# Optimization experiments

Hardware: AMD Instinct MI355X
Metric: run time of the kernel (lower is better)

Reference implementation:

```python
import jax, jax.numpy as jnp
import numpy as np

K = 3
BN_EPS = 1e-3


def setup_inputs() -> dict:
    key = jax.random.key(0)
    ks = jax.random.split(key, 13)
    B, N1, N2 = 8, 1024, 4096
    C1, C2, Cs = 256, 128, 64
    Ctot = C1 + C2 + Cs  # 448
    H = 256
    return {
        "points1": jax.random.normal(ks[0], (B, 3, N1), jnp.float32),
        "points2": jax.random.normal(ks[1], (B, 3, N2), jnp.float32),
        "features1": jax.random.normal(ks[2], (B, C1, N1), jnp.float32),
        "features2": jax.random.normal(ks[3], (B, C2, N2), jnp.float32),
        "skip_features": jax.random.normal(ks[4], (B, Cs, N2), jnp.float32),
        # 1x1 Conv2d weights are equivalent to dense matrices [out, in]
        "W1": jax.random.normal(ks[5], (H, Ctot), jnp.float32) * 0.05,
        "b1": jax.random.normal(ks[6], (H,), jnp.float32) * 0.05,
        "g1": 1.0 + jax.random.normal(ks[7], (H,), jnp.float32) * 0.05,
        "beta1": jax.random.normal(ks[8], (H,), jnp.float32) * 0.05,
        "W2": jax.random.normal(ks[9], (H, H), jnp.float32) * 0.05,
        "b2": jax.random.normal(ks[10], (H,), jnp.float32) * 0.05,
        "g2": 1.0 + jax.random.normal(ks[11], (H,), jnp.float32) * 0.05,
        "beta2": jax.random.normal(ks[12], (H,), jnp.float32) * 0.05,
    }


def _conv_bn_relu(x, W, b, g, beta):
    # x: [B, N, Cin]; 1x1 conv == dense matmul per point
    y = jnp.einsum("bnc,oc->bno", x, W) + b
    # BatchNorm2d in training mode: batch stats over (batch, spatial) per channel
    mu = jnp.mean(y, axis=(0, 1))
    var = jnp.mean(jnp.square(y - mu), axis=(0, 1))  # biased variance
    y = (y - mu) * jax.lax.rsqrt(var + BN_EPS) * g + beta
    return jax.nn.relu(y)


def reference(points1, points2, features1, features2, skip_features,
              W1, b1, g1, beta1, W2, b2, g2, beta2):
    p1 = jnp.swapaxes(points1, 1, 2)  # [B, N1, 3]
    p2 = jnp.swapaxes(points2, 1, 2)  # [B, N2, 3]
    # pairwise Euclidean distances [B, N2, N1]
    d2 = (jnp.sum(p2 * p2, -1, keepdims=True)
          + jnp.sum(p1 * p1, -1)[:, None, :]
          - 2.0 * jnp.einsum("bnd,bmd->bnm", p2, p1))
    dist = jnp.sqrt(jnp.maximum(d2, 0.0))
    # k smallest distances
    neg_top, ind = jax.lax.top_k(-dist, K)  # ind: [B, N2, K]
    dk = -neg_top
    inv = 1.0 / (dk + 1e-10)
    w = inv / jnp.sum(inv, -1, keepdims=True)  # [B, N2, K]
    f1 = jnp.swapaxes(features1, 1, 2)  # [B, N1, C1]
    gathered = jax.vmap(lambda f, i: f[i])(f1, ind)  # [B, N2, K, C1]
    new = jnp.einsum("bnkc,bnk->bnc", gathered, w)  # inverse-distance interp
    x = jnp.concatenate([new,
                         jnp.swapaxes(features2, 1, 2),
                         jnp.swapaxes(skip_features, 1, 2)], axis=-1)
    x = _conv_bn_relu(x, W1, b1, g1, beta1)
    x = _conv_bn_relu(x, W2, b2, g2, beta2)
    return jnp.swapaxes(x, 1, 2)  # [B, Cout, N2]
```

## Files before the change

kernel.cpp:

```cpp
#include <hip/hip_runtime.h>
#include <cstdint>
#include <cstddef>

#define B_    8
#define N1_   1024
#define N2_   4096
#define C1_   256
#define C2_   128
#define CS_   64
#define CT_   448
#define H_    256
#define ROWS_ (B_ * N2_)
#define XW_   192

typedef __attribute__((ext_vector_type(8))) short bf16x8;
typedef __attribute__((ext_vector_type(4))) float f32x4;
typedef unsigned short ushort_t;
typedef unsigned int   uint_t;

__device__ __forceinline__ ushort_t f2bf(float f) {
    uint_t u = __float_as_uint(f);
    u = (u + 0x7fffu + ((u >> 16) & 1u)) >> 16;
    return (ushort_t)u;
}
__device__ __forceinline__ float bf2f(ushort_t h) {
    return __uint_as_float(((uint_t)h) << 16);
}
__device__ __forceinline__ void glds16(const void* g, void* l) {
    __builtin_amdgcn_global_load_lds(
        (const __attribute__((address_space(1))) void*)g,
        (__attribute__((address_space(3))) void*)l, 16, 0, 0);
}

__device__ __forceinline__ void tile_decode(int d, int& m0, int& n0) {
    const int j = d >> 3;
    m0 = ((d & 7) * 32 + (j >> 2)) * 128;
    n0 = (j & 3) * 64;
}

__global__ __launch_bounds__(256) void fused_pre(
    const float* __restrict__ p1, const float* __restrict__ p2,
    int* __restrict__ ind, float* __restrict__ wout,
    const float* __restrict__ f1, const float* __restrict__ f2,
    const float* __restrict__ fs, const float* __restrict__ W1,
    const float* __restrict__ W2, ushort_t* __restrict__ f1t,
    ushort_t* __restrict__ x, ushort_t* __restrict__ W1b, ushort_t* __restrict__ W2b)
{
#pragma clang fp contract(off)
    __shared__ __align__(16) char smem[32000];
    const int t = threadIdx.x;
    const int bid = blockIdx.x;
    if (bid < 1024) {
        float4*   cand  = (float4*)(smem);
        float*    pvals = (float*)(smem + 16512);
        float*    thr   = (float*)(smem + 19584);
        ushort_t* lists = (ushort_t*)(smem + 19712);
        float*    pdd   = (float*)(smem + 25856);
        int*      pdi   = (int*)(smem + 28928);
        const int b  = bid >> 7;
        const int qb = (bid & 127) * 32;
        const float* pb1 = p1 + (size_t)b * 3 * N1_;
        for (int i = t; i < N1_; i += 256) {
            float X = pb1[i], Y = pb1[N1_ + i], Z = pb1[2 * N1_ + i];
            cand[i] = make_float4(X, Y, Z, (X * X + Y * Y) + Z * Z);
        }
        const int q = t & 31, split = t >> 5;
        const int n = qb + q;
        const float* pb2 = p2 + (size_t)b * 3 * N2_;
        const float ax = pb2[n], ay = pb2[N2_ + n], az = pb2[2 * N2_ + n];
        const float s2a = (ax * ax + ay * ay) + az * az;
        const float m2x = -2.0f * ax, m2y = -2.0f * ay, m2z = -2.0f * az;
        __syncthreads();
        const int ibeg = split * 128, iend = ibeg + 128;
        {
            float a0 = 3e38f, a1 = 3e38f, a2 = 3e38f;
            for (int i = ibeg; i < iend; ++i) {
                float4 c = cand[i];
                float fd = fmaf(c.x, m2x, fmaf(c.y, m2y, fmaf(c.z, m2z, s2a + c.w)));
                float o0 = a0, o1 = a1;
                a0 = fminf(o0, fd);
                a1 = __builtin_amdgcn_fmed3f(fd, o0, o1);
                a2 = __builtin_amdgcn_fmed3f(fd, o1, a2);
            }
            pvals[t * 3 + 0] = a0; pvals[t * 3 + 1] = a1; pvals[t * 3 + 2] = a2;
        }
        __syncthreads();
        if (t < 32) {
            float m0 = 3e38f, m1 = 3e38f, m2v = 3e38f;
#pragma unroll
            for (int g = 0; g < 8; ++g)
#pragma unroll
                for (int r = 0; r < 3; ++r) {
                    float v = pvals[(g * 32 + t) * 3 + r];
                    float o0 = m0, o1 = m1;
                    m0 = fminf(o0, v);
                    m1 = __builtin_amdgcn_fmed3f(v, o0, o1);
                    m2v = __builtin_amdgcn_fmed3f(v, o1, m2v);
                }
            thr[t] = m2v + 2e-3f;
        }
        __syncthreads();
        const float th = thr[q];
        ushort_t* mylist = lists + (q * 8 + split) * 12;
        int cnt = 0;
        for (int i = ibeg; i < iend; ++i) {
            float4 c = cand[i];
            float fd = fmaf(c.x, m2x, fmaf(c.y, m2y, fmaf(c.z, m2z, s2a + c.w)));
            if (fd <= th && cnt < 12) { mylist[cnt] = (ushort_t)i; cnt++; }
        }
        float e0 = 3e38f, e1 = 3e38f, e2 = 3e38f;
        int   j0 = 0, j1 = 0, j2 = 0;
        for (int k = 0; k < cnt; ++k) {
            const int i = mylist[k];
            float4 c = cand[i];
            float dot = (ax * c.x + ay * c.y) + az * c.z;
            float dd  = (s2a + c.w) - 2.0f * dot;
            float d   = sqrtf(fmaxf(dd, 0.0f));
            if (d < e0)      { e2 = e1; j2 = j1; e1 = e0; j1 = j0; e0 = d; j0 = i; }
            else if (d < e1) { e2 = e1; j2 = j1; e1 = d;  j1 = i; }
            else if (d < e2) { e2 = d;  j2 = i; }
        }
        pdd[(split * 32 + q) * 3 + 0] = e0; pdi[(split * 32 + q) * 3 + 0] = j0;
        pdd[(split * 32 + q) * 3 + 1] = e1; pdi[(split * 32 + q) * 3 + 1] = j1;
        pdd[(split * 32 + q) * 3 + 2] = e2; pdi[(split * 32 + q) * 3 + 2] = j2;
        __syncthreads();
        if (t < 32) {
            float f0 = 3e38f, f1v = 3e38f, f2v = 3e38f;
            int   k0 = 0, k1 = 0, k2 = 0;
#pragma unroll
            for (int g = 0; g < 8; ++g)
#pragma unroll
                for (int r = 0; r < 3; ++r) {
                    float d = pdd[(g * 32 + t) * 3 + r];
                    int   i = pdi[(g * 32 + t) * 3 + r];
                    if (d < f0)       { f2v = f1v; k2 = k1; f1v = f0; k1 = k0; f0 = d; k0 = i; }
                    else if (d < f1v) { f2v = f1v; k2 = k1; f1v = d;  k1 = i; }
                    else if (d < f2v) { f2v = d;  k2 = i; }
                }
            float inv0 = 1.0f / (f0 + 1e-10f);
            float inv1 = 1.0f / (f1v + 1e-10f);
            float inv2 = 1.0f / (f2v + 1e-10f);
            float s = (inv0 + inv1) + inv2;
            const size_t row = (size_t)b * N2_ + qb + t;
            wout[row * 3 + 0] = inv0 / s;
            wout[row * 3 + 1] = inv1 / s;
            wout[row * 3 + 2] = inv2 / s;
            ind[row * 3 + 0] = k0;
            ind[row * 3 + 1] = k1;
            ind[row * 3 + 2] = k2;
        }
    } else if (bid < 1536) {
        float (*tile)[65] = (float (*)[65])smem;
        const int bid2 = bid - 1024;
        const int b  = bid2 >> 6;
        const int ct = (bid2 >> 4) & 3;
        const int nt = bid2 & 15;
        const int c0 = ct * 64, n0 = nt * 64;
        const float* src = f1 + ((size_t)b * C1_ + c0) * N1_ + n0;
#pragma unroll
        for (int j = 0; j < 16; ++j) {
            int lin = j * 256 + t;
            int ci = lin >> 6, nj = lin & 63;
            tile[ci][nj] = src[(size_t)ci * N1_ + nj];
        }
        __syncthreads();
        ushort_t* dst = f1t + ((size_t)b * N1_ + n0) * C1_ + c0;
#pragma unroll
        for (int j = 0; j < 8; ++j) {
            int lin = j * 256 + t;
            int ni = lin >> 5, cjp = (lin & 31) * 2;
            uint_t u = (uint_t)f2bf(tile[cjp][ni]) | ((uint_t)f2bf(tile[cjp + 1][ni]) << 16);
            *(uint_t*)&dst[(size_t)ni * C1_ + cjp] = u;
        }
    } else if (bid < 3072) {
        float (*tile)[65] = (float (*)[65])smem;
        const int bid2 = bid - 1536;
        const int b   = bid2 / 192;
        const int rem = bid2 - b * 192;
        const int ct  = rem >> 6;
        const int nt  = rem & 63;
        const float* src;
        if (ct < 2) src = f2 + ((size_t)b * C2_ + ct * 64) * N2_;
        else        src = fs + (size_t)b * CS_ * N2_;
        const int coff = ct * 64;
        const int n0 = nt * 64;
#pragma unroll
        for (int j = 0; j < 16; ++j) {
            int lin = j * 256 + t;
            int ci = lin >> 6, nj = lin & 63;
            tile[ci][nj] = src[(size_t)ci * N2_ + n0 + nj];
        }
        __syncthreads();
#pragma unroll
        for (int j = 0; j < 8; ++j) {
            int lin = j * 256 + t;
            int ni = lin >> 5, cjp = (lin & 31) * 2;
            uint_t u = (uint_t)f2bf(tile[cjp][ni]) | ((uint_t)f2bf(tile[cjp + 1][ni]) << 16);
            *(uint_t*)&x[((size_t)b * N2_ + n0 + ni) * XW_ + coff + cjp] = u;
        }
    } else {
        const int i = (bid - 3072) * 256 + t;
        if (i < H_ * CT_) W1b[i] = f2bf(W1[i]);
        if (i < H_ * H_)  W2b[i] = f2bf(W2[i]);
    }
}

__global__ __launch_bounds__(256, 4) void gemm1_fused(
    const ushort_t* __restrict__ f1t, const int* __restrict__ ind,
    const float* __restrict__ wgt, const ushort_t* __restrict__ x2,
    const ushort_t* __restrict__ Bw, const float* __restrict__ bias,
    ushort_t* __restrict__ C, float* __restrict__ ssum, float* __restrict__ ssq)
{
    __shared__ __align__(16) ushort_t smem[12288];
    ushort_t* As = smem;
    ushort_t* Bs = smem + 8192;
    ushort_t* Cs = smem;
    const int t = threadIdx.x;
    int m0, n0;
    tile_decode(blockIdx.x, m0, n0);
    const int lane = t & 63;
    const int wv = t >> 6;
    const int wrow = wv & 1, wcol = wv >> 1;
    const int lm = lane & 15, lq = lane >> 4;
    const int lrow8  = lane >> 3;
    const int lchunk = (lane & 7) ^ lrow8;
    const int aswz = lm & 7;
    const ushort_t* gB = Bw + (size_t)(n0 + wv * 16 + lrow8) * CT_ + lchunk * 8;
    ushort_t* lB = Bs + wv * 1024;
    const ushort_t* gA = x2 + (size_t)(m0 + wv * 32 + lrow8) * XW_ + lchunk * 8;
    ushort_t* lA = As + wv * 2048;
    const int arow  = t >> 1;
    const int acolc = (t & 1) * 4;
    const size_t grow = (size_t)m0 + arow;
    const int bb_ = (int)(grow >> 12);
    const int* ip = ind + grow * 3;
    const float* wp = wgt + grow * 3;
    const ushort_t* fb = f1t + (size_t)bb_ * N1_ * C1_;
    const ushort_t* ga0 = fb + (size_t)ip[0] * C1_ + acolc * 8;
    const ushort_t* ga1 = fb + (size_t)ip[1] * C1_ + acolc * 8;
    const ushort_t* ga2 = fb + (size_t)ip[2] * C1_ + acolc * 8;
    const float w0 = wp[0], w1 = wp[1], w2 = wp[2];
    ushort_t* awr = As + arow * 64;
    const int arsw = arow & 7;
    f32x4 acc[4][2];
#pragma unroll
    for (int i = 0; i < 4; ++i)
#pragma unroll
        for (int j = 0; j < 2; ++j)
            acc[i][j] = (f32x4){0.f, 0.f, 0.f, 0.f};

    for (int k0 = 0; k0 < CT_; k0 += 64) {
        __syncthreads();
        if (k0 < 256) {
#pragma unroll
            for (int g = 0; g < 4; ++g) {
                uint4 va = *(const uint4*)(ga0 + k0 + g * 8);
                uint4 vb = *(const uint4*)(ga1 + k0 + g * 8);
                uint4 vc = *(const uint4*)(ga2 + k0 + g * 8);
                const uint_t* pa = (const uint_t*)&va;
                const uint_t* pb = (const uint_t*)&vb;
                const uint_t* pc = (const uint_t*)&vc;
                uint_t o[4];
#pragma unroll
                for (int e = 0; e < 4; ++e) {
                    float lo = w0 * bf2f((ushort_t)(pa[e] & 0xffff))
                             + w1 * bf2f((ushort_t)(pb[e] & 0xffff))
                             + w2 * bf2f((ushort_t)(pc[e] & 0xffff));
                    float hi = w0 * bf2f((ushort_t)(pa[e] >> 16))
                             + w1 * bf2f((ushort_t)(pb[e] >> 16))
                             + w2 * bf2f((ushort_t)(pc[e] >> 16));
                    o[e] = (uint_t)f2bf(lo) | ((uint_t)f2bf(hi) << 16);
                }
                *(uint4*)&awr[((acolc + g) ^ arsw) * 8] = *(uint4*)o;
            }
        } else {
#pragma unroll
            for (int g = 0; g < 4; ++g)
                glds16(gA + (k0 - 256) + g * 8 * XW_, lA + g * 512);
        }
#pragma unroll
        for (int g = 0; g < 2; ++g)
            glds16(gB + k0 + g * 8 * CT_, lB + g * 512);
        __syncthreads();
#pragma unroll
        for (int h = 0; h < 2; ++h) {
            bf16x8 af[4], bfr[2];
#pragma unroll
            for (int i = 0; i < 4; ++i)
                af[i] = *(const bf16x8*)&As[(wrow * 64 + i * 16 + lm) * 64
                                            + (((h * 4 + lq) ^ aswz)) * 8];
#pragma unroll
            for (int j = 0; j < 2; ++j)
                bfr[j] = *(const bf16x8*)&Bs[(wcol * 32 + j * 16 + lm) * 64
                                             + (((h * 4 + lq) ^ aswz)) * 8];
#pragma unroll
            for (int i = 0; i < 4; ++i)
#pragma unroll
                for (int j = 0; j < 2; ++j)
                    acc[i][j] = __builtin_amdgcn_mfma_f32_16x16x32_bf16(af[i], bfr[j], acc[i][j], 0, 0, 0);
        }
    }
    __syncthreads();
#pragma unroll
    for (int j = 0; j < 2; ++j) {
        const int gn_l = wcol * 32 + j * 16 + lm;
        const int gn   = n0 + gn_l;
        const float bb = bias[gn];
        float ps = 0.0f, pq = 0.0f;
#pragma unroll
        for (int i = 0; i < 4; ++i) {
            const int row_l = wrow * 64 + i * 16 + lq * 4;
            f32x4 v = acc[i][j];
#pragma unroll
            for (int r = 0; r < 4; ++r) {
                float val = v[r] + bb;
                ps += val;
                pq += val * val;
                float vo = __shfl_xor(val, 1);
                uint_t packed = (lm & 1)
                    ? ((uint_t)f2bf(vo)  | ((uint_t)f2bf(val) << 16))
                    : ((uint_t)f2bf(val) | ((uint_t)f2bf(vo)  << 16));
                if ((lm & 1) == 0)
                    *(uint_t*)&Cs[(row_l + r) * 72 + (gn_l & ~1)] = packed;
            }
        }
        ps += __shfl_xor(ps, 16); pq += __shfl_xor(pq, 16);
        ps += __shfl_xor(ps, 32); pq += __shfl_xor(pq, 32);
        if (lane < 16) {
            atomicAdd(&ssum[gn], ps);
            atomicAdd(&ssq[gn], pq);
        }
    }
    __syncthreads();
    const int srow = t >> 3;
    const int scol = (t & 7) * 8;
#pragma unroll
    for (int rep = 0; rep < 4; ++rep) {
        const int row = srow + rep * 32;
        uint4 v = *(const uint4*)&Cs[row * 72 + scol];
        *(uint4*)(C + (size_t)(m0 + row) * H_ + n0 + scol) = v;
    }
}

__global__ __launch_bounds__(256, 4) void gemm2_fused(
    const ushort_t* __restrict__ A, const ushort_t* __restrict__ Bw,
    const float* __restrict__ bias,
    const float* __restrict__ s1, const float* __restrict__ q1,
    const float* __restrict__ g1, const float* __restrict__ be1,
    ushort_t* __restrict__ C, float* __restrict__ ssum, float* __restrict__ ssq)
{
    __shared__ __align__(16) ushort_t smem[15360];
    ushort_t* As0 = smem;
    ushort_t* As1 = smem + 5120;
    ushort_t* Bs  = smem + 10240;
    float*    sc  = (float*)(smem + 14336);
    float*    sh  = (float*)(smem + 14848);
    ushort_t* Cs  = smem;
    const int t = threadIdx.x;
    int m0, n0;
    tile_decode(blockIdx.x, m0, n0);
    const int lane = t & 63;
    const int wv = t >> 6;
    const int wrow = wv & 1, wcol = wv >> 1;
    const int lm = lane & 15, lq = lane >> 4;
    const int lrow8  = lane >> 3;
    const int lchunk = (lane & 7) ^ lrow8;
    const int aswz = lm & 7;
    const int arow = t >> 1, acol = (t & 1) * 32;
    {
        const float invN = 1.0f / (float)ROWS_;
        float mu  = s1[t] * invN;
        float var = q1[t] * invN - mu * mu;
        float s   = rsqrtf(var + 1e-3f) * g1[t];
        sc[t] = s;
        sh[t] = be1[t] - mu * s;
    }
    const ushort_t* gB = Bw + (size_t)(n0 + wv * 16 + lrow8) * H_ + lchunk * 8;
    ushort_t* lB = Bs + wv * 1024;
    const ushort_t* gA = A + (size_t)(m0 + arow) * H_ + acol;
    ushort_t* As_t = (t & 1) ? As1 : As0;
    f32x4 acc[4][2];
#pragma unroll
    for (int i = 0; i < 4; ++i)
#pragma unroll
        for (int j = 0; j < 2; ++j)
            acc[i][j] = (f32x4){0.f, 0.f, 0.f, 0.f};

    for (int k0 = 0; k0 < H_; k0 += 64) {
        uint4 av[4];
#pragma unroll
        for (int g = 0; g < 4; ++g)
            av[g] = *(const uint4*)(gA + k0 + g * 8);
        __syncthreads();
#pragma unroll
        for (int g = 0; g < 2; ++g)
            glds16(gB + k0 + g * 8 * H_, lB + g * 512);
#pragma unroll
        for (int g = 0; g < 4; ++g) {
            const uint_t* wsrc = (const uint_t*)&av[g];
            uint_t o[4];
#pragma unroll
            for (int e = 0; e < 4; ++e) {
                const int cb = k0 + acol + g * 8 + 2 * e;
                float lo = __uint_as_float(wsrc[e] << 16);
                float hi = __uint_as_float(wsrc[e] & 0xffff0000u);
                float r0 = fmaxf(fmaf(lo, sc[cb],     sh[cb]),     0.0f);
                float r1 = fmaxf(fmaf(hi, sc[cb + 1], sh[cb + 1]), 0.0f);
                o[e] = (uint_t)f2bf(r0) | ((uint_t)f2bf(r1) << 16);
            }
            *(uint4*)&As_t[arow * 40 + g * 8] = *(uint4*)o;
        }
        __syncthreads();
#pragma unroll
        for (int h = 0; h < 2; ++h) {
            const ushort_t* Ah = h ? As1 : As0;
            bf16x8 af[4], bfr[2];
#pragma unroll
            for (int i = 0; i < 4; ++i)
                af[i] = *(const bf16x8*)&Ah[(wrow * 64 + i * 16 + lm) * 40 + lq * 8];
#pragma unroll
            for (int j = 0; j < 2; ++j)
                bfr[j] = *(const bf16x8*)&Bs[(wcol * 32 + j * 16 + lm) * 64
                                             + (((h * 4 + lq) ^ aswz)) * 8];
#pragma unroll
            for (int i = 0; i < 4; ++i)
#pragma unroll
                for (int j = 0; j < 2; ++j)
                    acc[i][j] = __builtin_amdgcn_mfma_f32_16x16x32_bf16(af[i], bfr[j], acc[i][j], 0, 0, 0);
        }
    }
    __syncthreads();
#pragma unroll
    for (int j = 0; j < 2; ++j) {
        const int gn_l = wcol * 32 + j * 16 + lm;
        const int gn   = n0 + gn_l;
        const float bb = bias[gn];
        float ps = 0.0f, pq = 0.0f;
#pragma unroll
        for (int i = 0; i < 4; ++i) {
            const int row_l = wrow * 64 + i * 16 + lq * 4;
            f32x4 v = acc[i][j];
#pragma unroll
            for (int r = 0; r < 4; ++r) {
                float val = v[r] + bb;
                ps += val;
                pq += val * val;
                float vo = __shfl_xor(val, 1);
                uint_t packed = (lm & 1)
                    ? ((uint_t)f2bf(vo)  | ((uint_t)f2bf(val) << 16))
                    : ((uint_t)f2bf(val) | ((uint_t)f2bf(vo)  << 16));
                if ((lm & 1) == 0)
                    *(uint_t*)&Cs[(row_l + r) * 72 + (gn_l & ~1)] = packed;
            }
        }
        ps += __shfl_xor(ps, 16); pq += __shfl_xor(pq, 16);
        ps += __shfl_xor(ps, 32); pq += __shfl_xor(pq, 32);
        if (lane < 16) {
            atomicAdd(&ssum[gn], ps);
            atomicAdd(&ssq[gn], pq);
        }
    }
    __syncthreads();
    const int srow = t >> 3;
    const int scol = (t & 7) * 8;
#pragma unroll
    for (int rep = 0; rep < 4; ++rep) {
        const int row = srow + rep * 32;
        uint4 v = *(const uint4*)&Cs[row * 72 + scol];
        *(uint4*)(C + (size_t)(m0 + row) * H_ + n0 + scol) = v;
    }
}

__global__ __launch_bounds__(256) void bn_out_kernel(
    const ushort_t* __restrict__ y, const float* __restrict__ ssum, const float* __restrict__ ssq,
    const float* __restrict__ g, const float* __restrict__ beta, float* __restrict__ out)
{
    __shared__ float tile[64][65];
    __shared__ float sc[64], sh[64];
    const float invN = 1.0f / (float)ROWS_;
    const int bid = blockIdx.x;
    const int b  = bid >> 8;
    const int nt = (bid >> 2) & 63;
    const int ot = bid & 3;
    const int t = threadIdx.x;
    if (t < 64) {
        int c = ot * 64 + t;
        float mu  = ssum[c] * invN;
        float var = ssq[c] * invN - mu * mu;
        float s   = rsqrtf(var + 1e-3f) * g[c];
        sc[t] = s;
        sh[t] = beta[c] - mu * s;
    }
    __syncthreads();
    const int n0 = nt * 64, o0 = ot * 64;
    const ushort_t* yb = y + ((size_t)b * N2_ + n0) * H_ + o0;
#pragma unroll
    for (int j = 0; j < 8; ++j) {
        int lin = j * 256 + t;
        int nl = lin >> 5, cu = (lin & 31) * 2;
        uint_t u = *(const uint_t*)&yb[(size_t)nl * H_ + cu];
        tile[nl][cu]     = fmaxf(bf2f((ushort_t)(u & 0xffff)) * sc[cu]     + sh[cu],     0.0f);
        tile[nl][cu + 1] = fmaxf(bf2f((ushort_t)(u >> 16))    * sc[cu + 1] + sh[cu + 1], 0.0f);
    }
    __syncthreads();
    float* ob = out + ((size_t)b * H_ + o0) * N2_ + n0;
#pragma unroll
    for (int j = 0; j < 16; ++j) {
        int lin = j * 256 + t;
        int ol = lin >> 6, nl = lin & 63;
        ob[(size_t)ol * N2_ + nl] = tile[nl][ol];
    }
}

extern "C" void kernel_launch(void* const* d_in, const int* in_sizes, int n_in,
                              void* d_out, int out_size, void* d_ws, size_t ws_size,
                              hipStream_t stream)
{
    (void)in_sizes; (void)n_in; (void)out_size; (void)ws_size;
    const float* points1   = (const float*)d_in[0];
    const float* points2   = (const float*)d_in[1];
    const float* features1 = (const float*)d_in[2];
    const float* features2 = (const float*)d_in[3];
    const float* skipf     = (const float*)d_in[4];
    const float* W1  = (const float*)d_in[5];
    const float* b1  = (const float*)d_in[6];
    const float* g1  = (const float*)d_in[7];
    const float* be1 = (const float*)d_in[8];
    const float* W2  = (const float*)d_in[9];
    const float* b2  = (const float*)d_in[10];
    const float* g2  = (const float*)d_in[11];
    const float* be2 = (const float*)d_in[12];
    float* out = (float*)d_out;

    char* ws = (char*)d_ws;
    float*    s1  = (float*)(ws + 0);
    float*    q1  = (float*)(ws + 1024);
    float*    s2  = (float*)(ws + 2048);
    float*    q2  = (float*)(ws + 3072);
    int*      ind = (int*)(ws + 4096);
    float*    wgt = (float*)(ws + 397312);
    ushort_t* x   = (ushort_t*)(ws + 790528);
    ushort_t* y1b = (ushort_t*)(ws + 30150656);
    ushort_t* W1b = (ushort_t*)(ws + 63705088);
    ushort_t* W2b = (ushort_t*)(ws + 63934464);
    ushort_t* f1t = (ushort_t*)(ws + 64065536);
    ushort_t* y2b = x;

    hipMemsetAsync(ws, 0, 4096, stream);

    fused_pre<<<dim3(3520), dim3(256), 0, stream>>>(points1, points2, ind, wgt,
                                                    features1, features2, skipf,
                                                    W1, W2, f1t, x, W1b, W2b);

    gemm1_fused<<<dim3(ROWS_ / 128 * 4), dim3(256), 0, stream>>>(f1t, ind, wgt, x,
                                                                 W1b, b1, y1b, s1, q1);
    gemm2_fused<<<dim3(ROWS_ / 128 * 4), dim3(256), 0, stream>>>(y1b, W2b, b2, s1, q1, g1, be1, y2b, s2, q2);
    bn_out_kernel<<<dim3(2048), dim3(256), 0, stream>>>(y2b, s2, q2, g2, be2, out);
}
```

Before: 191.4 us.

## Double-buffer LDS tiles in gemm1_fused to overlap gather with MFMA

Adds ping-pong A/B shared-memory buffers to the fused first GEMM. The next K-tile's gathered feature loads and global-to-LDS copies are issued before the current tile's MFMAs, and the interpolation and LDS store happen afterwards. This cuts the loop to one barrier per iteration and hides gather latency. Shared memory doubles to 48KB and launch bounds drop from 4 to 3 blocks per CU, which lowers occupancy and raises register pressure from holding the prefetched vectors.

```diff
diff --git a/kernel.cpp b/kernel.cpp
--- a/kernel.cpp
+++ b/kernel.cpp
@@ -205,15 +205,13 @@
     }
 }
 
-__global__ __launch_bounds__(256, 4) void gemm1_fused(
+__global__ __launch_bounds__(256, 3) void gemm1_fused(
     const ushort_t* __restrict__ f1t, const int* __restrict__ ind,
     const float* __restrict__ wgt, const ushort_t* __restrict__ x2,
     const ushort_t* __restrict__ Bw, const float* __restrict__ bias,
     ushort_t* __restrict__ C, float* __restrict__ ssum, float* __restrict__ ssq)
 {
-    __shared__ __align__(16) ushort_t smem[12288];
-    ushort_t* As = smem;
-    ushort_t* Bs = smem + 8192;
+    __shared__ __align__(16) ushort_t smem[24576];
     ushort_t* Cs = smem;
     const int t = threadIdx.x;
     int m0, n0;
@@ -226,9 +224,7 @@
     const int lchunk = (lane & 7) ^ lrow8;
     const int aswz = lm & 7;
     const ushort_t* gB = Bw + (size_t)(n0 + wv * 16 + lrow8) * CT_ + lchunk * 8;
-    ushort_t* lB = Bs + wv * 1024;
     const ushort_t* gA = x2 + (size_t)(m0 + wv * 32 + lrow8) * XW_ + lchunk * 8;
-    ushort_t* lA = As + wv * 2048;
     const int arow  = t >> 1;
     const int acolc = (t & 1) * 4;
     const size_t grow = (size_t)m0 + arow;
@@ -240,8 +236,8 @@
     const ushort_t* ga1 = fb + (size_t)ip[1] * C1_ + acolc * 8;
     const ushort_t* ga2 = fb + (size_t)ip[2] * C1_ + acolc * 8;
     const float w0 = wp[0], w1 = wp[1], w2 = wp[2];
-    ushort_t* awr = As + arow * 64;
     const int arsw = arow & 7;
+    const int awoff = arow * 64;
     f32x4 acc[4][2];
 #pragma unroll
     for (int i = 0; i < 4; ++i)
@@ -249,17 +245,84 @@
         for (int j = 0; j < 2; ++j)
             acc[i][j] = (f32x4){0.f, 0.f, 0.f, 0.f};
 
-    for (int k0 = 0; k0 < CT_; k0 += 64) {
-        __syncthreads();
-        if (k0 < 256) {
+    {
+        ushort_t* A0 = smem;
+        ushort_t* B0 = smem + 16384;
+#pragma unroll
+        for (int g = 0; g < 4; ++g) {
+            uint4 va = *(const uint4*)(ga0 + g * 8);
+            uint4 vb = *(const uint4*)(ga1 + g * 8);
+            uint4 vc = *(const uint4*)(ga2 + g * 8);
+            const uint_t* pa = (const uint_t*)&va;
+            const uint_t* pb = (const uint_t*)&vb;
+            const uint_t* pc = (const uint_t*)&vc;
+            uint_t o[4];
+#pragma unroll
+            for (int e = 0; e < 4; ++e) {
+                float lo = w0 * bf2f((ushort_t)(pa[e] & 0xffff))
+                         + w1 * bf2f((ushort_t)(pb[e] & 0xffff))
+                         + w2 * bf2f((ushort_t)(pc[e] & 0xffff));
+                float hi = w0 * bf2f((ushort_t)(pa[e] >> 16))
+                         + w1 * bf2f((ushort_t)(pb[e] >> 16))
+                         + w2 * bf2f((ushort_t)(pc[e] >> 16));
+                o[e] = (uint_t)f2bf(lo) | ((uint_t)f2bf(hi) << 16);
+            }
+            *(uint4*)&A0[awoff + (((acolc + g) ^ arsw)) * 8] = *(uint4*)o;
+        }
+#pragma unroll
+        for (int g = 0; g < 2; ++g)
+            glds16(gB + g * 8 * CT_, B0 + wv * 1024 + g * 512);
+    }
+    __syncthreads();
+
+    for (int k = 0; k < 7; ++k) {
+        const int cu = k & 1;
+        const int k0n = k * 64 + 64;
+        ushort_t* Ac  = smem + (cu ? 8192 : 0);
+        ushort_t* Bc  = smem + 16384 + (cu ? 4096 : 0);
+        ushort_t* Anx = smem + (cu ? 0 : 8192);
+        ushort_t* Bnx = smem + 16384 + (cu ? 0 : 4096);
+        uint4 va[4], vb[4], vc[4];
+        if (k < 3) {
 #pragma unroll
             for (int g = 0; g < 4; ++g) {
-                uint4 va = *(const uint4*)(ga0 + k0 + g * 8);
-                uint4 vb = *(const uint4*)(ga1 + k0 + g * 8);
-                uint4 vc = *(const uint4*)(ga2 + k0 + g * 8);
-                const uint_t* pa = (const uint_t*)&va;
-                const uint_t* pb = (const uint_t*)&vb;
-                const uint_t* pc = (const uint_t*)&vc;
+                va[g] = *(const uint4*)(ga0 + k0n + g * 8);
+                vb[g] = *(const uint4*)(ga1 + k0n + g * 8);
+                vc[g] = *(const uint4*)(ga2 + k0n + g * 8);
+            }
+        } else if (k < 6) {
+#pragma unroll
+            for (int g = 0; g < 4; ++g)
+                glds16(gA + (k0n - 256) + g * 8 * XW_, Anx + wv * 2048 + g * 512);
+        }
+        if (k < 6) {
+#pragma unroll
+            for (int g = 0; g < 2; ++g)
+                glds16(gB + k0n + g * 8 * CT_, Bnx + wv * 1024 + g * 512);
+        }
+#pragma unroll
+        for (int h = 0; h < 2; ++h) {
+            bf16x8 af[4], bfr[2];
+#pragma unroll
+            for (int i = 0; i < 4; ++i)
+                af[i] = *(const bf16x8*)&Ac[(wrow * 64 + i * 16 + lm) * 64
+                                            + (((h * 4 + lq) ^ aswz)) * 8];
+#pragma unroll
+            for (int j = 0; j < 2; ++j)
+                bfr[j] = *(const bf16x8*)&Bc[(wcol * 32 + j * 16 + lm) * 64
+                                             + (((h * 4 + lq) ^ aswz)) * 8];
+#pragma unroll
+            for (int i = 0; i < 4; ++i)
+#pragma unroll
+                for (int j = 0; j < 2; ++j)
+                    acc[i][j] = __builtin_amdgcn_mfma_f32_16x16x32_bf16(af[i], bfr[j], acc[i][j], 0, 0, 0);
+        }
+        if (k < 3) {
+#pragma unroll
+            for (int g = 0; g < 4; ++g) {
+                const uint_t* pa = (const uint_t*)&va[g];
+                const uint_t* pb = (const uint_t*)&vb[g];
+                const uint_t* pc = (const uint_t*)&vc[g];
                 uint_t o[4];
 #pragma unroll
                 for (int e = 0; e < 4; ++e) {
@@ -271,35 +334,12 @@
                              + w2 * bf2f((ushort_t)(pc[e] >> 16));
                     o[e] = (uint_t)f2bf(lo) | ((uint_t)f2bf(hi) << 16);
                 }
-                *(uint4*)&awr[((acolc + g) ^ arsw) * 8] = *(uint4*)o;
-            }
-        } else {
-#pragma unroll
-            for (int g = 0; g < 4; ++g)
-                glds16(gA + (k0 - 256) + g * 8 * XW_, lA + g * 512);
-        }
-#pragma unroll
-        for (int g = 0; g < 2; ++g)
-            glds16(gB + k0 + g * 8 * CT_, lB + g * 512);
-        __syncthreads();
-#pragma unroll
-        for (int h = 0; h < 2; ++h) {
-            bf16x8 af[4], bfr[2];
-#pragma unroll
-            for (int i = 0; i < 4; ++i)
-                af[i] = *(const bf16x8*)&As[(wrow * 64 + i * 16 + lm) * 64
-                                            + (((h * 4 + lq) ^ aswz)) * 8];
-#pragma unroll
-            for (int j = 0; j < 2; ++j)
-                bfr[j] = *(const bf16x8*)&Bs[(wcol * 32 + j * 16 + lm) * 64
-                                             + (((h * 4 + lq) ^ aswz)) * 8];
-#pragma unroll
-            for (int i = 0; i < 4; ++i)
-#pragma unroll
-                for (int j = 0; j < 2; ++j)
-                    acc[i][j] = __builtin_amdgcn_mfma_f32_16x16x32_bf16(af[i], bfr[j], acc[i][j], 0, 0, 0);
-        }
-    }
+                *(uint4*)&Anx[awoff + (((acolc + g) ^ arsw)) * 8] = *(uint4*)o;
+            }
+        }
+        __syncthreads();
+    }
+
     __syncthreads();
 #pragma unroll
     for (int j = 0; j < 2; ++j) {
```

Result: no change. 193.1 us (+0.9%).

## Retile gemm1 to 64-row blocks spanning all 256 output columns

Applied to the files above, without the earlier changes.

Each gemm1 block now covers 64 rows by the full 256 output channels, where before it covered 128 rows by 64 columns. Before, each row's interpolated features (a gather from three neighbours plus a weighted sum) were recomputed by four column blocks; now they are computed once per row, removing redundant gather traffic and ALU work. In exchange, each block loads the whole W1 k-slice per step, LDS use grows, the accumulator set doubles (more register pressure) and the grid shape changes.

```diff
diff --git a/kernel.cpp b/kernel.cpp
--- a/kernel.cpp
+++ b/kernel.cpp
@@ -211,49 +211,47 @@
     const ushort_t* __restrict__ Bw, const float* __restrict__ bias,
     ushort_t* __restrict__ C, float* __restrict__ ssum, float* __restrict__ ssq)
 {
-    __shared__ __align__(16) ushort_t smem[12288];
+    __shared__ __align__(16) ushort_t smem[20480];
     ushort_t* As = smem;
-    ushort_t* Bs = smem + 8192;
+    ushort_t* Bs = smem + 4096;
     ushort_t* Cs = smem;
     const int t = threadIdx.x;
-    int m0, n0;
-    tile_decode(blockIdx.x, m0, n0);
+    const int m0 = blockIdx.x * 64;
     const int lane = t & 63;
     const int wv = t >> 6;
-    const int wrow = wv & 1, wcol = wv >> 1;
     const int lm = lane & 15, lq = lane >> 4;
     const int lrow8  = lane >> 3;
     const int lchunk = (lane & 7) ^ lrow8;
     const int aswz = lm & 7;
-    const ushort_t* gB = Bw + (size_t)(n0 + wv * 16 + lrow8) * CT_ + lchunk * 8;
-    ushort_t* lB = Bs + wv * 1024;
-    const ushort_t* gA = x2 + (size_t)(m0 + wv * 32 + lrow8) * XW_ + lchunk * 8;
-    ushort_t* lA = As + wv * 2048;
-    const int arow  = t >> 1;
-    const int acolc = (t & 1) * 4;
+    const ushort_t* gB = Bw + (size_t)(wv * 64 + lrow8) * CT_ + lchunk * 8;
+    ushort_t* lB = Bs + wv * 4096;
+    const ushort_t* gA = x2 + (size_t)(m0 + wv * 16 + lrow8) * XW_ + lchunk * 8;
+    ushort_t* lA = As + wv * 1024;
+    const int arow = t >> 2;
+    const int ac0  = (t & 3) * 2;
     const size_t grow = (size_t)m0 + arow;
     const int bb_ = (int)(grow >> 12);
     const int* ip = ind + grow * 3;
     const float* wp = wgt + grow * 3;
     const ushort_t* fb = f1t + (size_t)bb_ * N1_ * C1_;
-    const ushort_t* ga0 = fb + (size_t)ip[0] * C1_ + acolc * 8;
-    const ushort_t* ga1 = fb + (size_t)ip[1] * C1_ + acolc * 8;
-    const ushort_t* ga2 = fb + (size_t)ip[2] * C1_ + acolc * 8;
+    const ushort_t* ga0 = fb + (size_t)ip[0] * C1_ + ac0 * 8;
+    const ushort_t* ga1 = fb + (size_t)ip[1] * C1_ + ac0 * 8;
+    const ushort_t* ga2 = fb + (size_t)ip[2] * C1_ + ac0 * 8;
     const float w0 = wp[0], w1 = wp[1], w2 = wp[2];
     ushort_t* awr = As + arow * 64;
     const int arsw = arow & 7;
-    f32x4 acc[4][2];
+    f32x4 acc[4][4];
 #pragma unroll
     for (int i = 0; i < 4; ++i)
 #pragma unroll
-        for (int j = 0; j < 2; ++j)
+        for (int j = 0; j < 4; ++j)
             acc[i][j] = (f32x4){0.f, 0.f, 0.f, 0.f};
 
     for (int k0 = 0; k0 < CT_; k0 += 64) {
         __syncthreads();
         if (k0 < 256) {
 #pragma unroll
-            for (int g = 0; g < 4; ++g) {
+            for (int g = 0; g < 2; ++g) {
                 uint4 va = *(const uint4*)(ga0 + k0 + g * 8);
                 uint4 vb = *(const uint4*)(ga1 + k0 + g * 8);
                 uint4 vc = *(const uint4*)(ga2 + k0 + g * 8);
@@ -271,45 +269,44 @@
                              + w2 * bf2f((ushort_t)(pc[e] >> 16));
                     o[e] = (uint_t)f2bf(lo) | ((uint_t)f2bf(hi) << 16);
                 }
-                *(uint4*)&awr[((acolc + g) ^ arsw) * 8] = *(uint4*)o;
+                *(uint4*)&awr[((ac0 + g) ^ arsw) * 8] = *(uint4*)o;
             }
         } else {
 #pragma unroll
-            for (int g = 0; g < 4; ++g)
+            for (int g = 0; g < 2; ++g)
                 glds16(gA + (k0 - 256) + g * 8 * XW_, lA + g * 512);
         }
 #pragma unroll
-        for (int g = 0; g < 2; ++g)
+        for (int g = 0; g < 8; ++g)
             glds16(gB + k0 + g * 8 * CT_, lB + g * 512);
         __syncthreads();
 #pragma unroll
         for (int h = 0; h < 2; ++h) {
-            bf16x8 af[4], bfr[2];
+            bf16x8 af[4], bfr[4];
 #pragma unroll
             for (int i = 0; i < 4; ++i)
-                af[i] = *(const bf16x8*)&As[(wrow * 64 + i * 16 + lm) * 64
+                af[i] = *(const bf16x8*)&As[(i * 16 + lm) * 64
                                             + (((h * 4 + lq) ^ aswz)) * 8];
 #pragma unroll
-            for (int j = 0; j < 2; ++j)
-                bfr[j] = *(const bf16x8*)&Bs[(wcol * 32 + j * 16 + lm) * 64
+            for (int j = 0; j < 4; ++j)
+                bfr[j] = *(const bf16x8*)&Bs[(wv * 64 + j * 16 + lm) * 64
                                              + (((h * 4 + lq) ^ aswz)) * 8];
 #pragma unroll
             for (int i = 0; i < 4; ++i)
 #pragma unroll
-                for (int j = 0; j < 2; ++j)
+                for (int j = 0; j < 4; ++j)
                     acc[i][j] = __builtin_amdgcn_mfma_f32_16x16x32_bf16(af[i], bfr[j], acc[i][j], 0, 0, 0);
         }
     }
     __syncthreads();
 #pragma unroll
-    for (int j = 0; j < 2; ++j) {
-        const int gn_l = wcol * 32 + j * 16 + lm;
-        const int gn   = n0 + gn_l;
+    for (int j = 0; j < 4; ++j) {
+        const int gn = wv * 64 + j * 16 + lm;
         const float bb = bias[gn];
         float ps = 0.0f, pq = 0.0f;
 #pragma unroll
         for (int i = 0; i < 4; ++i) {
-            const int row_l = wrow * 64 + i * 16 + lq * 4;
+            const int row_l = i * 16 + lq * 4;
             f32x4 v = acc[i][j];
 #pragma unroll
             for (int r = 0; r < 4; ++r) {
@@ -321,7 +318,7 @@
                     ? ((uint_t)f2bf(vo)  | ((uint_t)f2bf(val) << 16))
                     : ((uint_t)f2bf(val) | ((uint_t)f2bf(vo)  << 16));
                 if ((lm & 1) == 0)
-                    *(uint_t*)&Cs[(row_l + r) * 72 + (gn_l & ~1)] = packed;
+                    *(uint_t*)&Cs[(row_l + r) * 264 + (gn & ~1)] = packed;
             }
         }
         ps += __shfl_xor(ps, 16); pq += __shfl_xor(pq, 16);
@@ -332,13 +329,13 @@
         }
     }
     __syncthreads();
-    const int srow = t >> 3;
-    const int scol = (t & 7) * 8;
-#pragma unroll
-    for (int rep = 0; rep < 4; ++rep) {
-        const int row = srow + rep * 32;
-        uint4 v = *(const uint4*)&Cs[row * 72 + scol];
-        *(uint4*)(C + (size_t)(m0 + row) * H_ + n0 + scol) = v;
+    const int srow = t >> 5;
+    const int scol = (t & 31) * 8;
+#pragma unroll
+    for (int rep = 0; rep < 8; ++rep) {
+        const int row = srow + rep * 8;
+        uint4 v = *(const uint4*)&Cs[row * 264 + scol];
+        *(uint4*)(C + (size_t)(m0 + row) * H_ + scol) = v;
     }
 }
 
@@ -552,8 +549,8 @@
                                                     features1, features2, skipf,
                                                     W1, W2, f1t, x, W1b, W2b);
 
-    gemm1_fused<<<dim3(ROWS_ / 128 * 4), dim3(256), 0, stream>>>(f1t, ind, wgt, x,
-                                                                 W1b, b1, y1b, s1, q1);
+    gemm1_fused<<<dim3(ROWS_ / 64), dim3(256), 0, stream>>>(f1t, ind, wgt, x,
+                                                            W1b, b1, y1b, s1, q1);
     gemm2_fused<<<dim3(ROWS_ / 128 * 4), dim3(256), 0, stream>>>(y1b, W2b, b2, s1, q1, g1, be1, y2b, s2, q2);
     bn_out_kernel<<<dim3(2048), dim3(256), 0, stream>>>(y2b, s2, q2, g2, be2, out);
 }
```

Result: no change. 189.3 us (median of 2 runs) (-1.1%).
